# Kernel tuning notes

Hardware: AMD Instinct MI355X
Metric: run time of the kernel (lower is better)

Reference implementation:

```python
import jax, jax.numpy as jnp
import numpy as np


def setup_inputs() -> dict:
    key = jax.random.key(0)
    ks = jax.random.split(key, 9)
    B, T, S, D = 4, 256, 256, 512
    scale = 1.0 / np.sqrt(D)
    inp = {
        "output": jax.random.normal(ks[0], (B, T, D), dtype=jnp.float32),
        "context": jax.random.normal(ks[1], (B, S, D), dtype=jnp.float32),
        "mask": jax.random.randint(ks[2], (B, S), 0, 2, dtype=jnp.int32),
        # learned params (nn.Linear stores y = x @ W.T + b; we store W.T directly)
        "Wq": jax.random.normal(ks[3], (D, D), dtype=jnp.float32) * scale,
        "bq": jax.random.normal(ks[4], (D,), dtype=jnp.float32) * scale,
        "Wc": jax.random.normal(ks[5], (D, D), dtype=jnp.float32) * scale,
        "v": jax.random.normal(ks[6], (D,), dtype=jnp.float32) * scale,
        "Wout": jax.random.normal(ks[7], (2 * D, D), dtype=jnp.float32) * scale,
        "bout": jax.random.normal(ks[8], (D,), dtype=jnp.float32) * scale,
    }
    return inp


def reference(output, context, mask, Wq, bq, Wc, v, Wout, bout):
    # output: (B, T, D) decoder states; context: (B, S, D) encoder states
    wq = jnp.einsum("btd,de->bte", output, Wq) + bq          # (B, T, D)
    uh = jnp.einsum("bsd,de->bse", context, Wc)               # (B, S, D)
    # additive score: v . tanh(wq + uh), broadcast over (T, S)
    wquh = jnp.tanh(wq[:, :, None, :] + uh[:, None, :, :])    # (B, T, S, D)
    score = jnp.einsum("btsd,d->bts", wquh, v)                # (B, T, S)
    # masked softmax exactly as the torch code: max over ALL positions,
    # then zero out masked entries (mask==1 means masked) and renormalize.
    max_by_row = jnp.max(score, axis=-1, keepdims=True)
    keep = (1.0 - mask.astype(score.dtype))[:, None, :]       # (B, 1, S)
    attn = jnp.exp(score - max_by_row) * keep
    attn = attn / jnp.sum(attn, axis=-1, keepdims=True)       # (B, T, S)
    mix = jnp.einsum("bts,bsd->btd", attn, context)           # (B, T, D)
    combined = jnp.concatenate([mix, output], axis=-1)        # (B, T, 2D)
    out = jnp.einsum("btf,fd->btd", combined, Wout) + bout    # (B, T, D)
    return out, attn
```

## Files before the change

kernel.cpp:

```cpp
#include <hip/hip_runtime.h>
#include <hip/hip_bf16.h>

#define B_ 4
#define T_ 256
#define S_ 256
#define D_ 512
#define TB 2

typedef __bf16 bf16x8 __attribute__((ext_vector_type(8)));
typedef float  floatx4 __attribute__((ext_vector_type(4)));

#define C2F 2.885390081777926f

static __device__ __forceinline__ unsigned short f2bf(float x) {
    __hip_bfloat16 h = __float2bfloat16(x);
    return *reinterpret_cast<unsigned short*>(&h);
}
static __device__ __forceinline__ float asf(unsigned int u) {
    float f; __builtin_memcpy(&f, &u, 4); return f;
}
static __device__ __forceinline__ float clamp_pos(float x) {
    return fminf(fmaxf(x, 1e-15f), 1e15f);
}


__global__ __launch_bounds__(256) void prep(
    const float* __restrict__ output, const float* __restrict__ context,
    const float* __restrict__ Wq, const float* __restrict__ Wc,
    const float* __restrict__ Wout,
    unsigned short* __restrict__ out_f, unsigned short* __restrict__ ctx_f,
    unsigned short* __restrict__ Wq_f, unsigned short* __restrict__ Wc_f,
    unsigned short* __restrict__ WoT_f, unsigned short* __restrict__ WoB_f)
{
    const int tid = threadIdx.x;
    const int z = blockIdx.z;

    if (z >= 4) {
        const float* src = (z == 4) ? output : context;
        unsigned short* dst = (z == 4) ? out_f : ctx_f;
        const int bid  = blockIdx.y * 16 + blockIdx.x;
        const int tile = bid * 4 + (tid >> 6);
        const int lane = tid & 63;
        const int mblk = tile >> 4, kblk = tile & 15;
        const float* s = src + (size_t)(mblk * 16 + (lane & 15)) * 512
                             + kblk * 32 + (lane >> 4) * 8;
        float4 a = *(const float4*)s;
        float4 b = *(const float4*)(s + 4);
        uint4 pk;
        pk.x = (unsigned)f2bf(a.x) | ((unsigned)f2bf(a.y) << 16);
        pk.y = (unsigned)f2bf(a.z) | ((unsigned)f2bf(a.w) << 16);
        pk.z = (unsigned)f2bf(b.x) | ((unsigned)f2bf(b.y) << 16);
        pk.w = (unsigned)f2bf(b.z) | ((unsigned)f2bf(b.w) << 16);
        *(uint4*)(dst + (size_t)tile * 512 + lane * 8) = pk;
        return;
    }

    const float* W; unsigned short* WF; int krow0;
    if      (z == 0) { W = Wq;   WF = Wq_f;  krow0 = 0;   }
    else if (z == 1) { W = Wc;   WF = Wc_f;  krow0 = 0;   }
    else if (z == 2) { W = Wout; WF = WoT_f; krow0 = 0;   }
    else             { W = Wout; WF = WoB_f; krow0 = 512; }

    const int n0 = blockIdx.x * 32;
    const int k0 = blockIdx.y * 32;

    __shared__ float tile[32][33];
    const int c = tid & 31, r = tid >> 5;
    #pragma unroll
    for (int i = 0; i < 4; ++i)
        tile[r + 8 * i][c] = W[(size_t)(krow0 + k0 + r + 8 * i) * 512 + n0 + c];
    __syncthreads();
    #pragma unroll
    for (int i = 0; i < 4; ++i) {
        const int n = n0 + r + 8 * i;
        const int k = k0 + c;
        const int tl = (n >> 4) * 16 + (k >> 5);
        const int ln = (n & 15) | (((k >> 3) & 3) << 4);
        WF[((size_t)tl * 64 + ln) * 8 + (k & 7)] = f2bf(tile[c][r + 8 * i]);
    }
}

struct GArgs {
    const unsigned short* Af;
    const unsigned short* Bf;
    const float* aux;
    void* C;
    int mode;
};

__global__ __launch_bounds__(256) void gemm2(GArgs g0, GArgs g1, GArgs g2, GArgs g3)
{
    const int z = blockIdx.z;
    GArgs g = (z == 0) ? g0 : (z == 1) ? g1 : (z == 2) ? g2 : g3;

    const int tid  = threadIdx.x;
    const int wave = tid >> 6, lane = tid & 63;
    const int l15  = lane & 15, quad = lane >> 4;
    const int mblk = blockIdx.y * 4 + wave;
    const int nb0  = blockIdx.x * 2;

    const unsigned short* Ap  = g.Af + ((size_t)mblk * 16 * 64 + lane) * 8;
    const unsigned short* Bp0 = g.Bf + ((size_t)nb0 * 16 * 64 + lane) * 8;
    const unsigned short* Bp1 = Bp0 + (size_t)16 * 64 * 8;

    floatx4 acc[2];
    acc[0] = (floatx4){0.f, 0.f, 0.f, 0.f};
    acc[1] = (floatx4){0.f, 0.f, 0.f, 0.f};

    #pragma unroll 4
    for (int k = 0; k < 16; ++k) {
        bf16x8 a  = *(const bf16x8*)(Ap  + k * 512);
        bf16x8 b0 = *(const bf16x8*)(Bp0 + k * 512);
        bf16x8 b1 = *(const bf16x8*)(Bp1 + k * 512);
        acc[0] = __builtin_amdgcn_mfma_f32_16x16x32_bf16(a, b0, acc[0], 0, 0, 0);
        acc[1] = __builtin_amdgcn_mfma_f32_16x16x32_bf16(a, b1, acc[1], 0, 0, 0);
    }

    #pragma unroll
    for (int ni = 0; ni < 2; ++ni) {
        const int col = (nb0 + ni) * 16 + l15;
        const int rbase = mblk * 16 + quad * 4;
        if (g.mode == 1) {
            float* Cf = (float*)g.C;
            float bv = g.aux[col];
            #pragma unroll
            for (int r = 0; r < 4; ++r) {
                float hh = __builtin_amdgcn_exp2f(C2F * (acc[ni][r] + bv));
                Cf[(size_t)(rbase + r) * 512 + col] = clamp_pos(hh);
            }
        } else if (g.mode == 3) {
            float* Cf = (float*)g.C;
            #pragma unroll
            for (int r = 0; r < 4; ++r) {
                int row = rbase + r, bb = row >> 8, ss = row & 255;
                float gg = __builtin_amdgcn_exp2f(-C2F * acc[ni][r]);
                Cf[((size_t)(bb * 128 + (col >> 2)) * 256 + ss) * 4 + (col & 3)]
                    = clamp_pos(gg);
            }
        } else if (g.mode == 5) {
            unsigned short* Cb = (unsigned short*)g.C;
            #pragma unroll
            for (int r = 0; r < 4; ++r)
                Cb[(size_t)(rbase + r) * 512 + col] = f2bf(acc[ni][r]);
        } else {
            float* Cf = (float*)g.C;
            float bv = g.aux[col];
            #pragma unroll
            for (int r = 0; r < 4; ++r)
                Cf[(size_t)(rbase + r) * 512 + col] = acc[ni][r] + bv;
        }
    }
}

__global__ __launch_bounds__(1024) void attn_fused(
    const float* __restrict__ Hb,
    const float* __restrict__ Gb,
    const unsigned short* __restrict__ CWb,
    const float* __restrict__ OB,
    const int*   __restrict__ mask,
    const float* __restrict__ v,
    float* __restrict__ attn_out,
    float* __restrict__ out)
{
    const int bg  = blockIdx.x;
    const int b   = bg / (T_ / TB);
    const int t0  = (bg % (T_ / TB)) * TB;
    const int tid = threadIdx.x;
    const int s   = tid & 255;
    const int h   = tid >> 8;

    __shared__ float  w_s[TB][D_];
    __shared__ float  v_s[D_];
    __shared__ float2 part[4][256];
    __shared__ float2 wred[4];
    __shared__ float  a_s[TB][256];
    __shared__ float  mixp[4][TB][D_];

    if (tid < 512) {
        w_s[0][tid] = Hb[(size_t)(b * T_ + t0 + 0) * D_ + tid];
        w_s[1][tid] = Hb[(size_t)(b * T_ + t0 + 1) * D_ + tid];
        v_s[tid]    = v[tid];
    }
    __syncthreads();

    float acc0 = 0.f, acc1 = 0.f;
    const float* gbase = Gb + ((size_t)(b * 128 + h * 32) * 256 + s) * 4;

    #pragma unroll 4
    for (int dd = 0; dd < 16; ++dd) {
        float4 ga = *(const float4*)(gbase + dd * 2048);
        float4 gb = *(const float4*)(gbase + dd * 2048 + 1024);
        const int dbase = (h * 16 + dd) * 8;
        float4 va  = *(const float4*)&v_s[dbase];
        float4 vb  = *(const float4*)&v_s[dbase + 4];
        float4 h0a = *(const float4*)&w_s[0][dbase];
        float4 h0b = *(const float4*)&w_s[0][dbase + 4];
        float4 h1a = *(const float4*)&w_s[1][dbase];
        float4 h1b = *(const float4*)&w_s[1][dbase + 4];
        float G[8]  = {ga.x,  ga.y,  ga.z,  ga.w,  gb.x,  gb.y,  gb.z,  gb.w};
        float V[8]  = {va.x,  va.y,  va.z,  va.w,  vb.x,  vb.y,  vb.z,  vb.w};
        float H0[8] = {h0a.x, h0a.y, h0a.z, h0a.w, h0b.x, h0b.y, h0b.z, h0b.w};
        float H1[8] = {h1a.x, h1a.y, h1a.z, h1a.w, h1b.x, h1b.y, h1b.z, h1b.w};
        #pragma unroll
        for (int p = 0; p < 4; ++p) {
            float G0 = G[2 * p], G1 = G[2 * p + 1];
            float P0 = V[2 * p] * G0, P1 = V[2 * p + 1] * G1;
            float D00 = G0 + H0[2 * p], D01 = G1 + H0[2 * p + 1];
            acc0 = fmaf(fmaf(P0, D01, P1 * D00),
                        __builtin_amdgcn_rcpf(D00 * D01), acc0);
            float D10 = G0 + H1[2 * p], D11 = G1 + H1[2 * p + 1];
            acc1 = fmaf(fmaf(P0, D11, P1 * D10),
                        __builtin_amdgcn_rcpf(D10 * D11), acc1);
        }
    }
    part[h][s] = make_float2(acc0, acc1);
    __syncthreads();

    float p0 = 0.f, p1 = 0.f;
    if (tid < 256) {
        float A0 = part[0][tid].x + part[1][tid].x + part[2][tid].x + part[3][tid].x;
        float A1 = part[0][tid].y + part[1][tid].y + part[2][tid].y + part[3][tid].y;
        float keep = 1.0f - (float)mask[b * S_ + tid];
        p0 = __builtin_amdgcn_exp2f(-C2F * A0) * keep;
        p1 = __builtin_amdgcn_exp2f(-C2F * A1) * keep;
        float s0 = p0, s1 = p1;
        #pragma unroll
        for (int off = 1; off < 64; off <<= 1) {
            s0 += __shfl_xor(s0, off);
            s1 += __shfl_xor(s1, off);
        }
        if ((tid & 63) == 0) wred[tid >> 6] = make_float2(s0, s1);
    }
    __syncthreads();

    if (tid < 256) {
        float den0 = wred[0].x + wred[1].x + wred[2].x + wred[3].x;
        float den1 = wred[0].y + wred[1].y + wred[2].y + wred[3].y;
        float a0 = p0 * __builtin_amdgcn_rcpf(den0);
        float a1 = p1 * __builtin_amdgcn_rcpf(den1);
        attn_out[(size_t)(b * T_ + t0 + 0) * S_ + tid] = a0;
        attn_out[(size_t)(b * T_ + t0 + 1) * S_ + tid] = a1;
        a_s[0][tid] = a0;
        a_s[1][tid] = a1;
    }
    __syncthreads();

    const int d2 = tid & 255;
    const int sh = h * 64;
    const unsigned short* cw = CWb + ((size_t)(b * S_) + sh) * D_ + 2 * d2;
    float m[TB][2] = {};
    #pragma unroll 8
    for (int s2 = 0; s2 < 64; ++s2) {
        unsigned int cc = *(const unsigned int*)(cw + (size_t)s2 * D_);
        float c0 = asf(cc << 16), c1 = asf(cc & 0xffff0000u);
        #pragma unroll
        for (int t = 0; t < TB; ++t) {
            float a = a_s[t][sh + s2];
            m[t][0] = fmaf(a, c0, m[t][0]);
            m[t][1] = fmaf(a, c1, m[t][1]);
        }
    }
    #pragma unroll
    for (int t = 0; t < TB; ++t) {
        mixp[h][t][2 * d2]     = m[t][0];
        mixp[h][t][2 * d2 + 1] = m[t][1];
    }
    __syncthreads();

    {
        const int t = tid >> 9, d = tid & 511;
        size_t idx = (size_t)(b * T_ + t0 + t) * D_ + d;
        out[idx] = mixp[0][t][d] + mixp[1][t][d] + mixp[2][t][d] + mixp[3][t][d]
                 + OB[idx];
    }
}

extern "C" void kernel_launch(void* const* d_in, const int* in_sizes, int n_in,
                              void* d_out, int out_size, void* d_ws, size_t ws_size,
                              hipStream_t stream) {
    const float* output  = (const float*)d_in[0];
    const float* context = (const float*)d_in[1];
    const int*   mask    = (const int*)d_in[2];
    const float* Wq      = (const float*)d_in[3];
    const float* bq      = (const float*)d_in[4];
    const float* Wc      = (const float*)d_in[5];
    const float* v       = (const float*)d_in[6];
    const float* Wout    = (const float*)d_in[7];
    const float* bout    = (const float*)d_in[8];

    float* out  = (float*)d_out;
    float* attn = out + (size_t)B_ * T_ * D_;

    char* ws = (char*)d_ws;
    float* Hb             = (float*)ws;
    float* OB             = (float*)(ws + (2u << 20));
    float* Gb             = (float*)(ws + (4u << 20));
    unsigned short* out_f = (unsigned short*)(ws + (6u << 20));
    unsigned short* ctx_f = (unsigned short*)(ws + (7u << 20));
    unsigned short* Wq_f  = (unsigned short*)(ws + (8u << 20));
    unsigned short* Wc_f  = (unsigned short*)(ws + (8u << 20) + (512u << 10));
    unsigned short* WoT_f = (unsigned short*)(ws + (9u << 20));
    unsigned short* WoB_f = (unsigned short*)(ws + (9u << 20) + (512u << 10));
    unsigned short* CWb   = (unsigned short*)(ws + (10u << 20));

    dim3 blk(256);

    prep<<<dim3(16, 16, 6), blk, 0, stream>>>(
        output, context, Wq, Wc, Wout, out_f, ctx_f, Wq_f, Wc_f, WoT_f, WoB_f);

    GArgs gwq = { out_f, Wq_f,  bq,      Hb,  1 };
    GArgs guh = { ctx_f, Wc_f,  nullptr, Gb,  3 };
    GArgs gob = { out_f, WoB_f, bout,    OB,  4 };
    GArgs gcw = { ctx_f, WoT_f, nullptr, CWb, 5 };
    gemm2<<<dim3(16, 16, 4), blk, 0, stream>>>(gwq, guh, gob, gcw);

    attn_fused<<<dim3(B_ * T_ / TB), dim3(1024), 0, stream>>>(
        Hb, Gb, CWb, OB, mask, v, attn, out);
}
```

Measured before the change: 119.8 us.

## Store context projection as bf16 exp/v ratio and simplify tanh-pair algebra

The context-projection GEMM epilogue now writes exp(2*uh)/v as bf16 in an 8-wide interleaved layout instead of fp32 exp(-2*uh). This halves the bytes the attention kernel streams for the dominant B*S*D operand and removes a multiply per pair in the inner score loop, using 1/v precomputed in shared memory. Block indices are also remapped so that consecutive launched blocks spread across batches and time positions. The bf16 rounding of the ratio and the reciprocal of v can lower accuracy, and small v values risk overflow; clamps are added to contain this.

```diff
diff --git a/kernel.cpp b/kernel.cpp
--- a/kernel.cpp
+++ b/kernel.cpp
@@ -129,13 +129,16 @@
                 Cf[(size_t)(rbase + r) * 512 + col] = clamp_pos(hh);
             }
         } else if (g.mode == 3) {
-            float* Cf = (float*)g.C;
+            unsigned short* Cb = (unsigned short*)g.C;
+            float rv = __builtin_amdgcn_rcpf(g.aux[col]);
+            rv = fminf(fmaxf(rv, -1e30f), 1e30f);
             #pragma unroll
             for (int r = 0; r < 4; ++r) {
                 int row = rbase + r, bb = row >> 8, ss = row & 255;
-                float gg = __builtin_amdgcn_exp2f(-C2F * acc[ni][r]);
-                Cf[((size_t)(bb * 128 + (col >> 2)) * 256 + ss) * 4 + (col & 3)]
-                    = clamp_pos(gg);
+                float ww = __builtin_amdgcn_exp2f(C2F * acc[ni][r]) * rv;
+                ww = fminf(fmaxf(ww, -1e20f), 1e20f);
+                Cb[((size_t)(bb * 64 + (col >> 3)) * 256 + ss) * 8 + (col & 7)]
+                    = f2bf(ww);
             }
         } else if (g.mode == 5) {
             unsigned short* Cb = (unsigned short*)g.C;
@@ -154,7 +157,7 @@
 
 __global__ __launch_bounds__(1024) void attn_fused(
     const float* __restrict__ Hb,
-    const float* __restrict__ Gb,
+    const unsigned short* __restrict__ Wb,
     const unsigned short* __restrict__ CWb,
     const float* __restrict__ OB,
     const int*   __restrict__ mask,
@@ -162,7 +165,8 @@
     float* __restrict__ attn_out,
     float* __restrict__ out)
 {
-    const int bg  = blockIdx.x;
+    const int bid = blockIdx.x;
+    const int bg  = (bid & 7) * (B_ * T_ / TB / 8) + (bid >> 3);
     const int b   = bg / (T_ / TB);
     const int t0  = (bg % (T_ / TB)) * TB;
     const int tid = threadIdx.x;
@@ -179,38 +183,41 @@
     if (tid < 512) {
         w_s[0][tid] = Hb[(size_t)(b * T_ + t0 + 0) * D_ + tid];
         w_s[1][tid] = Hb[(size_t)(b * T_ + t0 + 1) * D_ + tid];
-        v_s[tid]    = v[tid];
+        float iv = __builtin_amdgcn_rcpf(v[tid]);
+        v_s[tid] = fminf(fmaxf(iv, -1e30f), 1e30f);
     }
     __syncthreads();
 
     float acc0 = 0.f, acc1 = 0.f;
-    const float* gbase = Gb + ((size_t)(b * 128 + h * 32) * 256 + s) * 4;
+    const uint4* wb4 = (const uint4*)(Wb + ((size_t)(b * 64 + h * 16) * 256 + s) * 8);
 
     #pragma unroll 4
     for (int dd = 0; dd < 16; ++dd) {
-        float4 ga = *(const float4*)(gbase + dd * 2048);
-        float4 gb = *(const float4*)(gbase + dd * 2048 + 1024);
+        uint4 ww = wb4[(size_t)dd * 256];
+        float W[8];
+        W[0] = asf(ww.x << 16); W[1] = asf(ww.x & 0xffff0000u);
+        W[2] = asf(ww.y << 16); W[3] = asf(ww.y & 0xffff0000u);
+        W[4] = asf(ww.z << 16); W[5] = asf(ww.z & 0xffff0000u);
+        W[6] = asf(ww.w << 16); W[7] = asf(ww.w & 0xffff0000u);
+
         const int dbase = (h * 16 + dd) * 8;
-        float4 va  = *(const float4*)&v_s[dbase];
-        float4 vb  = *(const float4*)&v_s[dbase + 4];
+        float4 iva = *(const float4*)&v_s[dbase];
+        float4 ivb = *(const float4*)&v_s[dbase + 4];
         float4 h0a = *(const float4*)&w_s[0][dbase];
         float4 h0b = *(const float4*)&w_s[0][dbase + 4];
         float4 h1a = *(const float4*)&w_s[1][dbase];
         float4 h1b = *(const float4*)&w_s[1][dbase + 4];
-        float G[8]  = {ga.x,  ga.y,  ga.z,  ga.w,  gb.x,  gb.y,  gb.z,  gb.w};
-        float V[8]  = {va.x,  va.y,  va.z,  va.w,  vb.x,  vb.y,  vb.z,  vb.w};
+        float IV[8] = {iva.x, iva.y, iva.z, iva.w, ivb.x, ivb.y, ivb.z, ivb.w};
         float H0[8] = {h0a.x, h0a.y, h0a.z, h0a.w, h0b.x, h0b.y, h0b.z, h0b.w};
         float H1[8] = {h1a.x, h1a.y, h1a.z, h1a.w, h1b.x, h1b.y, h1b.z, h1b.w};
         #pragma unroll
         for (int p = 0; p < 4; ++p) {
-            float G0 = G[2 * p], G1 = G[2 * p + 1];
-            float P0 = V[2 * p] * G0, P1 = V[2 * p + 1] * G1;
-            float D00 = G0 + H0[2 * p], D01 = G1 + H0[2 * p + 1];
-            acc0 = fmaf(fmaf(P0, D01, P1 * D00),
-                        __builtin_amdgcn_rcpf(D00 * D01), acc0);
-            float D10 = G0 + H1[2 * p], D11 = G1 + H1[2 * p + 1];
-            acc1 = fmaf(fmaf(P0, D11, P1 * D10),
-                        __builtin_amdgcn_rcpf(D10 * D11), acc1);
+            float W0 = W[2 * p], W1 = W[2 * p + 1];
+            float i0 = IV[2 * p], i1 = IV[2 * p + 1];
+            float x00 = fmaf(H0[2 * p], W0, i0), x01 = fmaf(H0[2 * p + 1], W1, i1);
+            acc0 = fmaf(x00 + x01, __builtin_amdgcn_rcpf(x00 * x01), acc0);
+            float x10 = fmaf(H1[2 * p], W0, i0), x11 = fmaf(H1[2 * p + 1], W1, i1);
+            acc1 = fmaf(x10 + x11, __builtin_amdgcn_rcpf(x10 * x11), acc1);
         }
     }
     part[h][s] = make_float2(acc0, acc1);
@@ -294,7 +301,7 @@
     char* ws = (char*)d_ws;
     float* Hb             = (float*)ws;
     float* OB             = (float*)(ws + (2u << 20));
-    float* Gb             = (float*)(ws + (4u << 20));
+    unsigned short* Wb    = (unsigned short*)(ws + (4u << 20));
     unsigned short* out_f = (unsigned short*)(ws + (6u << 20));
     unsigned short* ctx_f = (unsigned short*)(ws + (7u << 20));
     unsigned short* Wq_f  = (unsigned short*)(ws + (8u << 20));
@@ -308,12 +315,12 @@
     prep<<<dim3(16, 16, 6), blk, 0, stream>>>(
         output, context, Wq, Wc, Wout, out_f, ctx_f, Wq_f, Wc_f, WoT_f, WoB_f);
 
-    GArgs gwq = { out_f, Wq_f,  bq,      Hb,  1 };
-    GArgs guh = { ctx_f, Wc_f,  nullptr, Gb,  3 };
-    GArgs gob = { out_f, WoB_f, bout,    OB,  4 };
-    GArgs gcw = { ctx_f, WoT_f, nullptr, CWb, 5 };
+    GArgs gwq = { out_f, Wq_f,  bq,   Hb,  1 };
+    GArgs guh = { ctx_f, Wc_f,  v,    Wb,  3 };
+    GArgs gob = { out_f, WoB_f, bout, OB,  4 };
+    GArgs gcw = { ctx_f, WoT_f, NULL, CWb, 5 };
     gemm2<<<dim3(16, 16, 4), blk, 0, stream>>>(gwq, guh, gob, gcw);
 
     attn_fused<<<dim3(B_ * T_ / TB), dim3(1024), 0, stream>>>(
-        Hb, Gb, CWb, OB, mask, v, attn, out);
-}
+        Hb, Wb, CWb, OB, mask, v, attn, out);
+}
```

Result: faster. 113.0 us (-5.7%).
